# Performance work log

Measured on AMD Instinct MI355X. Metric: run time of the kernel, lower is better.

Reference implementation:

```python
import jax, jax.numpy as jnp
import numpy as np

N_ENT, N_CON, DIM, R, NB = 30000, 29309, 128, 12, 8
B, LC, S, E_DB, E_CON = 256, 50, 32, 300000, 200000


def setup_inputs() -> dict:
    key = jax.random.key(0)
    ks = jax.random.split(key, 32)
    f = lambda k, sh: (jax.random.normal(k, sh, jnp.float32) * 0.02)
    concept_emb = f(ks[0], (N_CON, DIM)).at[0].set(0.0)  # padding_idx=0 row zeroed
    inp = {
        'concept_mask': jax.random.randint(ks[1], (B, LC), 0, N_CON, jnp.int32),
        'seed_pad': jax.random.randint(ks[2], (B, S), 0, N_ENT, jnp.int32),
        'seed_lens': jax.random.randint(ks[3], (B,), 0, S + 1, jnp.int32),
        'db_edge_index': jax.random.randint(ks[4], (2, E_DB), 0, N_ENT, jnp.int32),
        'db_edge_type': jax.random.randint(ks[5], (E_DB,), 0, R, jnp.int32),
        'con_edge_index': jax.random.randint(ks[6], (2, E_CON), 0, N_CON, jnp.int32),
        'db_vec': jax.random.uniform(ks[7], (B, N_ENT), jnp.float32),
        'labels': jax.random.randint(ks[8], (B,), 0, N_ENT, jnp.int64),
        'rec': jax.random.uniform(ks[9], (B,), jnp.float32),
        'concept_emb': concept_emb,
        'basis': f(ks[10], (NB, N_ENT, DIM)),
        'comp': f(ks[11], (R, NB)),
        'rgcn_root': f(ks[12], (N_ENT, DIM)),
        'rgcn_bias': jnp.zeros((DIM,), jnp.float32),
        'gcn_w': f(ks[13], (DIM, DIM)),
        'gcn_b': jnp.zeros((DIM,), jnp.float32),
        'attn_a': f(ks[14], (DIM, DIM)),
        'attn_b': f(ks[15], (DIM, 1)),
        'attn_a_db': f(ks[16], (DIM, DIM)),
        'attn_b_db': f(ks[17], (DIM, 1)),
        'user_norm_w': f(ks[18], (DIM, 2 * DIM)),
        'user_norm_b': jnp.zeros((DIM,), jnp.float32),
        'gate_norm_w': f(ks[19], (1, DIM)),
        'gate_norm_b': jnp.zeros((1,), jnp.float32),
        'info_con_w': f(ks[20], (DIM, DIM)),
        'info_con_b': jnp.zeros((DIM,), jnp.float32),
        'info_out_db_b': jnp.zeros((N_ENT,), jnp.float32),
        'output_en_b': jnp.zeros((N_ENT,), jnp.float32),
    }
    return inp


def _forward(concept_mask, seed_pad, seed_lens, db_edge_index, db_edge_type,
             con_edge_index, db_vec, labels, rec, concept_emb, basis, comp,
             rgcn_root, rgcn_bias, gcn_w, gcn_b, attn_a, attn_b, attn_a_db,
             attn_b_db, user_norm_w, user_norm_b, gate_norm_w, gate_norm_b,
             info_con_w, info_con_b, info_out_db_b, output_en_b):
    NEG = jnp.float32(-1e30)
    # ---- RGCN over DBpedia graph (x=None -> per-edge row W[rel][src]) ----
    w = jnp.einsum('rb,bnd->rnd', comp, basis)            # [R, N_ent, D]
    src, dst = db_edge_index[0], db_edge_index[1]
    msg = w[db_edge_type, src]                            # [E, D]
    agg = jax.ops.segment_sum(msg, dst, num_segments=N_ENT)
    cnt = jax.ops.segment_sum(jnp.ones_like(dst, jnp.float32), dst, num_segments=N_ENT)
    db_feats = agg / jnp.maximum(cnt, 1.0)[:, None] + rgcn_root + rgcn_bias  # mean aggr + root + bias
    # ---- GCN over concept graph (symmetric norm, self-loops) ----
    xw = concept_emb @ gcn_w
    loops = jnp.arange(N_CON, dtype=con_edge_index.dtype)
    cs = jnp.concatenate([con_edge_index[0], loops])
    cd = jnp.concatenate([con_edge_index[1], loops])
    deg = jax.ops.segment_sum(jnp.ones_like(cd, jnp.float32), cd, num_segments=N_CON)
    dinv = jnp.where(deg > 0, jax.lax.rsqrt(jnp.maximum(deg, 1e-12)), 0.0)
    norm = dinv[cs] * dinv[cd]
    con_feats = jax.ops.segment_sum(norm[:, None] * xw[cs], cd, num_segments=N_CON) + gcn_b
    # ---- per-sample seed-set self-attention over db features ----
    h = db_feats[seed_pad]                                # [B, S, D]
    e = jnp.tanh(h @ attn_a_db) @ attn_b_db               # [B, S, 1]
    valid = jnp.arange(S)[None, :] < seed_lens[:, None]   # [B, S]
    a = jax.nn.softmax(jnp.where(valid[..., None], e, NEG), axis=1)
    db_user = jnp.einsum('bso,bsd->bd', a, h)             # weighted sum (o=1)
    has_seed = (seed_lens > 0)
    db_user = jnp.where(has_seed[:, None], db_user, 0.0)  # empty seed set -> zeros
    db_con_mask = has_seed.astype(jnp.float32)
    # ---- batch self-attention over gathered concept features ----
    hc = con_feats[concept_mask]                          # [B, LC, D]
    ec = jnp.tanh(hc @ attn_a) @ attn_b                   # [B, LC, 1]
    cvalid = (concept_mask != 0)
    ac = jax.nn.softmax(jnp.where(cvalid[..., None], ec, NEG), axis=1)
    con_user = jnp.einsum('blo,bld->bd', ac, hc)
    # ---- gated fusion ----
    u = jnp.concatenate([con_user, db_user], axis=-1) @ user_norm_w.T + user_norm_b
    gate = jax.nn.sigmoid(u @ gate_norm_w.T + gate_norm_b)  # [B, 1]
    user_emb = gate * db_user + (1.0 - gate) * con_user
    entity_scores = user_emb @ db_feats.T + output_en_b   # [B, N_ent]
    # ---- infomax MSE loss ----
    con_e = con_user @ info_con_w.T + info_con_b
    db_scores = con_e @ db_feats.T + info_out_db_b
    info_db_loss = jnp.mean(jnp.sum((db_scores - db_vec) ** 2, axis=-1) * db_con_mask)
    # ---- rec CE loss ----
    logp = jax.nn.log_softmax(entity_scores, axis=-1)
    ce = -jnp.take_along_axis(logp, labels[:, None].astype(jnp.int32), axis=1)[:, 0]
    rec_loss = jnp.sum(ce * rec)
    loss = rec_loss + 0.025 * info_db_loss                # pretrain=False path
    return loss, entity_scores, rec_loss


def reference(concept_mask, seed_pad, seed_lens, db_edge_index, db_edge_type,
              con_edge_index, db_vec, labels, rec, concept_emb, basis, comp,
              rgcn_root, rgcn_bias, gcn_w, gcn_b, attn_a, attn_b, attn_a_db,
              attn_b_db, user_norm_w, user_norm_b, gate_norm_w, gate_norm_b,
              info_con_w, info_con_b, info_out_db_b, output_en_b):
    return _forward(concept_mask, seed_pad, seed_lens, db_edge_index, db_edge_type,
                    con_edge_index, db_vec, labels, rec, concept_emb, basis, comp,
                    rgcn_root, rgcn_bias, gcn_w, gcn_b, attn_a, attn_b, attn_a_db,
                    attn_b_db, user_norm_w, user_norm_b, gate_norm_w, gate_norm_b,
                    info_con_w, info_con_b, info_out_db_b, output_en_b)
```

## Files before the change

kernel.cpp:

```cpp
#include <hip/hip_runtime.h>

#define N_ENT  30000
#define N_CON  29309
#define DIM    128
#define NBASIS 8
#define NREL   12
#define BATCH  256
#define LCON   50
#define SSEED  32
#define EDB    300000
#define ECON   200000
#define NTILE  938

#define NE4      ((N_CON * DIM) / 4)
#define NB_HIST  ((EDB + ECON + 255) / 256)
#define NB_CONV  ((NE4 + 3 * (DIM * DIM / 4) + 255) / 256)
#define NB_WCOMP ((N_ENT * 32) / 256)
#define NB_XW    ((N_CON + 127) / 128)
#define NB_RG    ((N_ENT + 3) / 4)
#define NB_GG    ((N_CON + 3) / 4)
#define NB_EDB   ((N_ENT + 31) / 32)
#define NB_ECON  ((N_CON + 31) / 32)

typedef __attribute__((ext_vector_type(8)))  short bfrag8;
typedef __attribute__((ext_vector_type(16))) float facc16;

__device__ __forceinline__ unsigned short f2bf(float f) {
    unsigned int u = __float_as_uint(f);
    u += 0x7FFFu + ((u >> 16) & 1u);
    return (unsigned short)(u >> 16);
}
__device__ __forceinline__ float bf2f(unsigned int h) {
    return __uint_as_float(h << 16);
}

__global__ __launch_bounds__(256) void prep_kernel(const int* __restrict__ db_dst,
                                                   const int* __restrict__ con_dst,
                                                   const float* __restrict__ emb,
                                                   const float* __restrict__ W,
                                                   const float* __restrict__ A_db,
                                                   const float* __restrict__ A_c,
                                                   int* __restrict__ cnt_e, int* __restrict__ cnt_c,
                                                   int* __restrict__ ord_db, int* __restrict__ ord_con,
                                                   unsigned short* __restrict__ emb_h,
                                                   unsigned short* __restrict__ Wt_h,
                                                   unsigned short* __restrict__ At_db_h,
                                                   unsigned short* __restrict__ At_c_h) {
    int t = threadIdx.x, bb = blockIdx.x;
    if (bb < NB_HIST) {
        int e = bb * 256 + t;
        if (e < EDB) {
            ord_db[e] = atomicAdd(cnt_e + db_dst[e], 1);
        } else if (e < EDB + ECON) {
            int ee = e - EDB;
            ord_con[ee] = atomicAdd(cnt_c + con_dst[ee], 1);
        }
        return;
    }
    int i = (bb - NB_HIST) * 256 + t;
    if (i < NE4) {
        float4 v = ((const float4*)emb)[i];
        unsigned int p0 = (unsigned int)f2bf(v.x) | ((unsigned int)f2bf(v.y) << 16);
        unsigned int p1 = (unsigned int)f2bf(v.z) | ((unsigned int)f2bf(v.w) << 16);
        *(uint2*)(emb_h + (size_t)i * 4) = make_uint2(p0, p1);
    } else {
        int j = i - NE4;
        if (j < 3 * (DIM * DIM) / 4) {
            int sel = j >> 12;
            int jj = j & 4095;
            const float* S = (sel == 0) ? W : ((sel == 1) ? A_db : A_c);
            unsigned short* Dst = (sel == 0) ? Wt_h : ((sel == 1) ? At_db_h : At_c_h);
            int o = jj * 4;
            int n = o >> 7, k0 = o & 127;
            unsigned int p0 = (unsigned int)f2bf(S[(k0 + 0) * DIM + n]) |
                              ((unsigned int)f2bf(S[(k0 + 1) * DIM + n]) << 16);
            unsigned int p1 = (unsigned int)f2bf(S[(k0 + 2) * DIM + n]) |
                              ((unsigned int)f2bf(S[(k0 + 3) * DIM + n]) << 16);
            *(uint2*)(Dst + n * DIM + k0) = make_uint2(p0, p1);
        }
    }
}

__device__ void scan_block(const int* __restrict__ cnt, int n, int* __restrict__ rowptr) {
    __shared__ int part[1024];
    int t = threadIdx.x;
    int per = (n + 1023) / 1024;
    int s0 = t * per;
    int sum = 0;
    for (int i = 0; i < per; ++i) {
        int idx = s0 + i;
        if (idx < n) sum += cnt[idx];
    }
    part[t] = sum;
    __syncthreads();
    for (int off = 1; off < 1024; off <<= 1) {
        int v = (t >= off) ? part[t - off] : 0;
        __syncthreads();
        part[t] += v;
        __syncthreads();
    }
    int run = part[t] - sum;
    for (int i = 0; i < per; ++i) {
        int idx = s0 + i;
        if (idx < n) {
            rowptr[idx] = run;
            run += cnt[idx];
        }
    }
    if (t == 1023) rowptr[n] = part[1023];
}

__global__ __launch_bounds__(1024) void scan2_kernel(const int* __restrict__ cnt_e,
                                                     const int* __restrict__ cnt_c,
                                                     int* __restrict__ rowptr_e,
                                                     int* __restrict__ rowptr_c,
                                                     float* __restrict__ dinv,
                                                     const unsigned short* __restrict__ emb_h,
                                                     const unsigned short* __restrict__ Wt_h,
                                                     unsigned short* __restrict__ xw_h) {
    int bb = blockIdx.x;
    if (bb == 0) {
        scan_block(cnt_e, N_ENT, rowptr_e);
        return;
    }
    if (bb == 1) {
        scan_block(cnt_c, N_CON, rowptr_c);
        for (int i = threadIdx.x; i < N_CON; i += 1024)
            dinv[i] = rsqrtf((float)(cnt_c[i] + 1));
        return;
    }
    int t = threadIdx.x;
    int wave = t >> 6, lane = t & 63;
    int m0 = (bb - 2) * 128 + (wave >> 2) * 32;
    int n0 = (wave & 3) * 32;
    int am = lane & 31, ak = (lane >> 5) * 8;
    int mrow = m0 + am;
    bool mv = mrow < N_CON;
    const unsigned short* Ar = emb_h + (size_t)mrow * DIM + ak;
    const unsigned short* Br = Wt_h + (size_t)(n0 + am) * DIM + ak;
    facc16 acc;
#pragma unroll
    for (int r = 0; r < 16; ++r) acc[r] = 0.f;
#pragma unroll
    for (int s = 0; s < 8; ++s) {
        bfrag8 a;
#pragma unroll
        for (int j = 0; j < 8; ++j) a[j] = 0;
        if (mv) a = *(const bfrag8*)(Ar + s * 16);
        bfrag8 b = *(const bfrag8*)(Br + s * 16);
        acc = __builtin_amdgcn_mfma_f32_32x32x16_bf16(a, b, acc, 0, 0, 0);
    }
    int col = lane & 31;
    int g4 = (lane >> 5) * 4;
#pragma unroll
    for (int r = 0; r < 16; ++r) {
        int m = m0 + (r & 3) + ((r >> 2) << 3) + g4;
        if (m < N_CON) xw_h[(size_t)m * DIM + n0 + col] = f2bf(acc[r]);
    }
}

__global__ __launch_bounds__(256) void scatter_kernel(const int* __restrict__ db_eidx,
                                                      const int* __restrict__ db_etype,
                                                      const int* __restrict__ con_eidx,
                                                      const int* __restrict__ ord_db,
                                                      const int* __restrict__ ord_con,
                                                      const int* __restrict__ rowptr_e,
                                                      const int* __restrict__ rowptr_c,
                                                      int* __restrict__ elist_e,
                                                      int* __restrict__ elist_c) {
    int e = blockIdx.x * 256 + threadIdx.x;
    if (e < EDB) {
        int dst = db_eidx[EDB + e];
        elist_e[rowptr_e[dst] + ord_db[e]] = db_eidx[e] | (db_etype[e] << 18);
    } else if (e < EDB + ECON) {
        int ee = e - EDB;
        int dst = con_eidx[ECON + ee];
        elist_c[rowptr_c[dst] + ord_con[ee]] = con_eidx[ee];
    }
}

__global__ __launch_bounds__(256) void wcomp_gcn_kernel(const float* __restrict__ basis,
                                                        const float* __restrict__ comp,
                                                        unsigned short* __restrict__ w_h,
                                                        int use_w,
                                                        const int* __restrict__ rowptr_c,
                                                        const int* __restrict__ elist_c,
                                                        const float* __restrict__ dinv,
                                                        const unsigned short* __restrict__ xw_h,
                                                        const float* __restrict__ gcn_b,
                                                        unsigned short* __restrict__ conf_h) {
    int t = threadIdx.x, bb = blockIdx.x;
    if (bb < NB_WCOMP) {
        __shared__ float sc[NREL * NBASIS];
        if (!use_w) return;
        if (t < NREL * NBASIS) sc[t] = comp[t];
        __syncthreads();
        int i = bb * 256 + t;
        int n = i >> 5, d4 = i & 31;
        float4 bv[NBASIS];
#pragma unroll
        for (int b = 0; b < NBASIS; ++b)
            bv[b] = ((const float4*)(basis + ((size_t)b * N_ENT + n) * DIM))[d4];
#pragma unroll
        for (int r = 0; r < NREL; ++r) {
            float4 acc = make_float4(0.f, 0.f, 0.f, 0.f);
#pragma unroll
            for (int b = 0; b < NBASIS; ++b) {
                float c = sc[r * NBASIS + b];
                acc.x += c * bv[b].x; acc.y += c * bv[b].y;
                acc.z += c * bv[b].z; acc.w += c * bv[b].w;
            }
            unsigned int p0 = (unsigned int)f2bf(acc.x) | ((unsigned int)f2bf(acc.y) << 16);
            unsigned int p1 = (unsigned int)f2bf(acc.z) | ((unsigned int)f2bf(acc.w) << 16);
            *(uint2*)(w_h + ((size_t)n * NREL + r) * DIM + d4 * 4) = make_uint2(p0, p1);
        }
        return;
    }
    int gb = bb - NB_WCOMP;
    int wid = gb * 4 + (t >> 6);
    if (wid >= N_CON) return;
    int lane = t & 63;
    int beg = rowptr_c[wid], end = rowptr_c[wid + 1];
    float a0 = 0.f, a1 = 0.f;
    int p = beg;
    for (; p + 3 < end; p += 4) {
        int s0 = elist_c[p], s1 = elist_c[p + 1], s2 = elist_c[p + 2], s3 = elist_c[p + 3];
        float n0 = dinv[s0], n1 = dinv[s1], n2 = dinv[s2], n3 = dinv[s3];
        unsigned int k0 = *(const unsigned int*)(xw_h + (size_t)s0 * DIM + lane * 2);
        unsigned int k1 = *(const unsigned int*)(xw_h + (size_t)s1 * DIM + lane * 2);
        unsigned int k2 = *(const unsigned int*)(xw_h + (size_t)s2 * DIM + lane * 2);
        unsigned int k3 = *(const unsigned int*)(xw_h + (size_t)s3 * DIM + lane * 2);
        a0 += n0 * bf2f(k0 & 0xFFFF) + n1 * bf2f(k1 & 0xFFFF) + n2 * bf2f(k2 & 0xFFFF) + n3 * bf2f(k3 & 0xFFFF);
        a1 += n0 * bf2f(k0 >> 16)    + n1 * bf2f(k1 >> 16)    + n2 * bf2f(k2 >> 16)    + n3 * bf2f(k3 >> 16);
    }
    for (; p < end; ++p) {
        int s = elist_c[p];
        float nm = dinv[s];
        unsigned int k = *(const unsigned int*)(xw_h + (size_t)s * DIM + lane * 2);
        a0 += nm * bf2f(k & 0xFFFF);
        a1 += nm * bf2f(k >> 16);
    }
    float dv = dinv[wid];
    unsigned int ks = *(const unsigned int*)(xw_h + (size_t)wid * DIM + lane * 2);
    size_t base = (size_t)wid * DIM + lane * 2;
    float f0 = dv * a0 + dv * dv * bf2f(ks & 0xFFFF) + gcn_b[lane * 2];
    float f1 = dv * a1 + dv * dv * bf2f(ks >> 16)    + gcn_b[lane * 2 + 1];
    *(unsigned int*)(conf_h + base) = (unsigned int)f2bf(f0) | ((unsigned int)f2bf(f1) << 16);
}

__device__ __forceinline__ void escore_body(const unsigned short* __restrict__ feats,
                                            const unsigned short* __restrict__ At,
                                            const float* __restrict__ v,
                                            float* __restrict__ eo,
                                            int m0, int nrow) {
    __shared__ float part[4][32];
    int t = threadIdx.x;
    int wave = t >> 6, lane = t & 63;
    int n0 = wave * 32;
    int am = lane & 31, ak = (lane >> 5) * 8;
    int mrow = m0 + am;
    bool mv = mrow < nrow;
    const unsigned short* Ar = feats + (size_t)mrow * DIM + ak;
    const unsigned short* Br = At + (size_t)(n0 + am) * DIM + ak;
    facc16 acc;
#pragma unroll
    for (int r = 0; r < 16; ++r) acc[r] = 0.f;
#pragma unroll
    for (int s = 0; s < 8; ++s) {
        bfrag8 a;
#pragma unroll
        for (int j = 0; j < 8; ++j) a[j] = 0;
        if (mv) a = *(const bfrag8*)(Ar + s * 16);
        bfrag8 b = *(const bfrag8*)(Br + s * 16);
        acc = __builtin_amdgcn_mfma_f32_32x32x16_bf16(a, b, acc, 0, 0, 0);
    }
    int col = lane & 31, g = lane >> 5;
    float vn = v[n0 + col];
#pragma unroll
    for (int r = 0; r < 16; ++r) {
        float x = tanhf(acc[r]) * vn;
#pragma unroll
        for (int off = 16; off >= 1; off >>= 1) x += __shfl_xor(x, off, 32);
        if (col == 0) {
            int row = (r & 3) + ((r >> 2) << 3) + (g << 2);
            part[wave][row] = x;
        }
    }
    __syncthreads();
    if (t < 32) {
        int m = m0 + t;
        if (m < nrow)
            eo[m] = part[0][t] + part[1][t] + part[2][t] + part[3][t];
    }
}

__global__ __launch_bounds__(256) void rgcn_escore_kernel(const int* __restrict__ rowptr_e,
                                                          const int* __restrict__ elist_e,
                                                          const unsigned short* __restrict__ w_h,
                                                          const float* __restrict__ root,
                                                          const float* __restrict__ bias,
                                                          unsigned short* __restrict__ dbf_h,
                                                          const unsigned short* __restrict__ conf_h,
                                                          const unsigned short* __restrict__ At_c_h,
                                                          const float* __restrict__ v_c,
                                                          float* __restrict__ e_con,
                                                          int use_w) {
    int bb = blockIdx.x;
    if (bb < NB_RG) {
        if (!use_w) return;
        int wid = bb * 4 + (threadIdx.x >> 6);
        int lane = threadIdx.x & 63;
        int beg = rowptr_e[wid], end = rowptr_e[wid + 1];
        float a0 = 0.f, a1 = 0.f;
        int p = beg;
        for (; p + 3 < end; p += 4) {
            int v0 = elist_e[p], v1 = elist_e[p + 1], v2 = elist_e[p + 2], v3 = elist_e[p + 3];
            unsigned int k0 = *(const unsigned int*)(w_h + ((size_t)(v0 & 0x3FFFF) * NREL + (v0 >> 18)) * DIM + lane * 2);
            unsigned int k1 = *(const unsigned int*)(w_h + ((size_t)(v1 & 0x3FFFF) * NREL + (v1 >> 18)) * DIM + lane * 2);
            unsigned int k2 = *(const unsigned int*)(w_h + ((size_t)(v2 & 0x3FFFF) * NREL + (v2 >> 18)) * DIM + lane * 2);
            unsigned int k3 = *(const unsigned int*)(w_h + ((size_t)(v3 & 0x3FFFF) * NREL + (v3 >> 18)) * DIM + lane * 2);
            a0 += bf2f(k0 & 0xFFFF) + bf2f(k1 & 0xFFFF) + bf2f(k2 & 0xFFFF) + bf2f(k3 & 0xFFFF);
            a1 += bf2f(k0 >> 16)    + bf2f(k1 >> 16)    + bf2f(k2 >> 16)    + bf2f(k3 >> 16);
        }
        for (; p < end; ++p) {
            int v = elist_e[p];
            unsigned int k = *(const unsigned int*)(w_h + ((size_t)(v & 0x3FFFF) * NREL + (v >> 18)) * DIM + lane * 2);
            a0 += bf2f(k & 0xFFFF);
            a1 += bf2f(k >> 16);
        }
        float inv = 1.f / fmaxf((float)(end - beg), 1.f);
        size_t base = (size_t)wid * DIM + lane * 2;
        float f0 = a0 * inv + root[base]     + bias[lane * 2];
        float f1 = a1 * inv + root[base + 1] + bias[lane * 2 + 1];
        *(unsigned int*)(dbf_h + base) = (unsigned int)f2bf(f0) | ((unsigned int)f2bf(f1) << 16);
        return;
    }
    escore_body(conf_h, At_c_h, v_c, e_con, (bb - NB_RG) * 32, N_CON);
}

__global__ __launch_bounds__(256) void rgcn_gather_basis(const int* __restrict__ rowptr,
                                                         const int* __restrict__ elist,
                                                         const float* __restrict__ basis,
                                                         const float* __restrict__ comp,
                                                         const float* __restrict__ root,
                                                         const float* __restrict__ bias,
                                                         unsigned short* __restrict__ dbf_h) {
    int wid  = blockIdx.x * 4 + (threadIdx.x >> 6);
    int lane = threadIdx.x & 63;
    if (wid >= N_ENT) return;
    int beg = rowptr[wid], end = rowptr[wid + 1];
    float a0 = 0.f, a1 = 0.f;
    for (int p = beg; p < end; ++p) {
        int v = elist[p];
        int src = v & 0x3FFFF, ty = v >> 18;
        const float* c = comp + ty * NBASIS;
#pragma unroll
        for (int b = 0; b < NBASIS; ++b) {
            const float* bp = basis + ((size_t)b * N_ENT + src) * DIM;
            a0 += c[b] * bp[lane * 2];
            a1 += c[b] * bp[lane * 2 + 1];
        }
    }
    float inv = 1.f / fmaxf((float)(end - beg), 1.f);
    size_t base = (size_t)wid * DIM + lane * 2;
    float f0 = a0 * inv + root[base]     + bias[lane * 2];
    float f1 = a1 * inv + root[base + 1] + bias[lane * 2 + 1];
    *(unsigned int*)(dbf_h + base) = (unsigned int)f2bf(f0) | ((unsigned int)f2bf(f1) << 16);
}

__global__ __launch_bounds__(256) void escore_db_kernel(const unsigned short* __restrict__ dbf_h,
                                                        const unsigned short* __restrict__ At_db_h,
                                                        const float* __restrict__ v_db,
                                                        float* __restrict__ e_db) {
    escore_body(dbf_h, At_db_h, v_db, e_db, blockIdx.x * 32, N_ENT);
}

__global__ __launch_bounds__(256) void attn_fusion_kernel(const unsigned short* __restrict__ dbf_h,
                                                          const unsigned short* __restrict__ conf_h,
                                                          const float* __restrict__ e_db,
                                                          const float* __restrict__ e_con,
                                                          const int* __restrict__ seed_pad,
                                                          const int* __restrict__ seed_lens,
                                                          const int* __restrict__ concept_mask,
                                                          const float* __restrict__ Wu, const float* __restrict__ bu,
                                                          const float* __restrict__ gw, const float* __restrict__ gb,
                                                          const float* __restrict__ Wi, const float* __restrict__ bi,
                                                          unsigned short* __restrict__ uemb_h,
                                                          unsigned short* __restrict__ cone_h,
                                                          float* __restrict__ maskv) {
    __shared__ int srow[SSEED];
    __shared__ int crow[LCON];
    __shared__ float a_db[SSEED], a_con[LCON];
    __shared__ float du[DIM], cu[DIM], red[DIM];
    int b = blockIdx.x, t = threadIdx.x;
    int wave = t >> 6, lane = t & 63;
    int len = seed_lens[b];
    if (wave == 0) {
        float e = -1e30f;
        if (lane < SSEED) {
            int rv = seed_pad[b * SSEED + lane];
            srow[lane] = rv;
            if (lane < len) e = e_db[rv];
        }
        float m = e;
#pragma unroll
        for (int off = 16; off >= 1; off >>= 1) m = fmaxf(m, __shfl_xor(m, off, 32));
        float p = (lane < SSEED) ? __expf(e - m) : 0.f;
        float s = p;
#pragma unroll
        for (int off = 16; off >= 1; off >>= 1) s += __shfl_xor(s, off, 32);
        if (lane < SSEED) a_db[lane] = p / s;
    } else if (wave == 1) {
        float e = -1e30f;
        if (lane < LCON) {
            int rv = concept_mask[b * LCON + lane];
            crow[lane] = rv;
            if (rv != 0) e = e_con[rv];
        }
        float m = e;
#pragma unroll
        for (int off = 32; off >= 1; off >>= 1) m = fmaxf(m, __shfl_xor(m, off, 64));
        float p = (lane < LCON) ? __expf(e - m) : 0.f;
        float s = p;
#pragma unroll
        for (int off = 32; off >= 1; off >>= 1) s += __shfl_xor(s, off, 64);
        if (lane < LCON) a_con[lane] = p / s;
    }
    __syncthreads();
    if (t < DIM) {
        float acc = 0.f;
#pragma unroll
        for (int s = 0; s < SSEED; ++s)
            acc += a_db[s] * bf2f((unsigned int)dbf_h[(size_t)srow[s] * DIM + t]);
        du[t] = (len > 0) ? acc : 0.f;
    } else {
        int d = t - DIM;
        float acc = 0.f;
#pragma unroll
        for (int s = 0; s < LCON; ++s)
            acc += a_con[s] * bf2f((unsigned int)conf_h[(size_t)crow[s] * DIM + d]);
        cu[d] = acc;
    }
    __syncthreads();
    if (t < DIM) {
        float u = bu[t];
        const float* wr = Wu + t * 2 * DIM;
        for (int k = 0; k < DIM; ++k) u += cu[k] * wr[k];
        for (int k = 0; k < DIM; ++k) u += du[k] * wr[DIM + k];
        red[t] = u * gw[t];
    }
    __syncthreads();
    for (int s2 = 64; s2 > 0; s2 >>= 1) {
        if (t < s2) red[t] += red[t + s2];
        __syncthreads();
    }
    if (t < DIM) {
        float gate = 1.f / (1.f + __expf(-(red[0] + gb[0])));
        uemb_h[b * DIM + t] = f2bf(gate * du[t] + (1.f - gate) * cu[t]);
        float ce = bi[t];
        const float* wi = Wi + t * DIM;
        for (int k = 0; k < DIM; ++k) ce += cu[k] * wi[k];
        cone_h[b * DIM + t] = f2bf(ce);
    }
    if (t == 0) maskv[b] = (len > 0) ? 1.f : 0.f;
}

__global__ __launch_bounds__(256) void score_mfma(const unsigned short* __restrict__ dbf_h,
                                                  const unsigned short* __restrict__ uemb_h,
                                                  const unsigned short* __restrict__ cone_h,
                                                  const float* __restrict__ en_b,
                                                  const float* __restrict__ info_b,
                                                  const float* __restrict__ db_vec,
                                                  float* __restrict__ escore,
                                                  float* __restrict__ partM,
                                                  float* __restrict__ partS,
                                                  float* __restrict__ partQ) {
    int wave = threadIdx.x >> 6, lane = threadIdx.x & 63;
    int nt = blockIdx.x * 4 + wave;
    if (nt >= NTILE) return;
    int b0 = blockIdx.y * 32;
    int n0 = nt * 32;
    int am = lane & 31, ak = (lane >> 5) * 8;
    int nb = n0 + am;
    bool bvalid = nb < N_ENT;
    const unsigned short* Au = uemb_h + (size_t)(b0 + am) * DIM + ak;
    const unsigned short* Ac = cone_h + (size_t)(b0 + am) * DIM + ak;
    const unsigned short* Bp = dbf_h + (size_t)nb * DIM + ak;
    facc16 accE, accD;
#pragma unroll
    for (int r = 0; r < 16; ++r) { accE[r] = 0.f; accD[r] = 0.f; }
#pragma unroll
    for (int s = 0; s < 8; ++s) {
        bfrag8 au = *(const bfrag8*)(Au + s * 16);
        bfrag8 ac = *(const bfrag8*)(Ac + s * 16);
        bfrag8 bb;
#pragma unroll
        for (int j = 0; j < 8; ++j) bb[j] = 0;
        if (bvalid) bb = *(const bfrag8*)(Bp + s * 16);
        accE = __builtin_amdgcn_mfma_f32_32x32x16_bf16(au, bb, accE, 0, 0, 0);
        accD = __builtin_amdgcn_mfma_f32_32x32x16_bf16(ac, bb, accD, 0, 0, 0);
    }
    int col = lane & 31;
    int n = n0 + col;
    bool nv = n < N_ENT;
    float enb = nv ? en_b[n] : 0.f;
    float inb = nv ? info_b[n] : 0.f;
    int g4 = (lane >> 5) * 4;
#pragma unroll
    for (int r = 0; r < 16; ++r) {
        int b = b0 + (r & 3) + ((r >> 2) << 3) + g4;
        float e = accE[r] + enb;
        if (nv) escore[(size_t)b * N_ENT + n] = e;
        float ev = nv ? e : -1e30f;
        float mx = ev;
#pragma unroll
        for (int off = 16; off >= 1; off >>= 1) mx = fmaxf(mx, __shfl_xor(mx, off, 64));
        float ex = nv ? __expf(e - mx) : 0.f;
        float sm = ex;
#pragma unroll
        for (int off = 16; off >= 1; off >>= 1) sm += __shfl_xor(sm, off, 64);
        float d = nv ? (accD[r] + inb - db_vec[(size_t)b * N_ENT + n]) : 0.f;
        float q = d * d;
#pragma unroll
        for (int off = 16; off >= 1; off >>= 1) q += __shfl_xor(q, off, 64);
        if (col == 0) {
            partM[(size_t)b * NTILE + nt] = mx;
            partS[(size_t)b * NTILE + nt] = sm;
            partQ[(size_t)b * NTILE + nt] = q;
        }
    }
}

__global__ __launch_bounds__(256) void ce_final(const float* __restrict__ partM,
                                                const float* __restrict__ partS,
                                                const float* __restrict__ partQ,
                                                const float* __restrict__ escore,
                                                const int* __restrict__ labels,
                                                const float* __restrict__ rec,
                                                float* __restrict__ rloss,
                                                float* __restrict__ ssqv) {
    __shared__ float red[256], red2[256];
    int b = blockIdx.x, t = threadIdx.x;
    const float* pm = partM + (size_t)b * NTILE;
    const float* ps = partS + (size_t)b * NTILE;
    const float* pq = partQ + (size_t)b * NTILE;
    float mx = -1e30f;
    for (int i = t; i < NTILE; i += 256) mx = fmaxf(mx, pm[i]);
    red[t] = mx;
    __syncthreads();
    for (int s2 = 128; s2 > 0; s2 >>= 1) {
        if (t < s2) red[t] = fmaxf(red[t], red[t + s2]);
        __syncthreads();
    }
    float M = red[0];
    __syncthreads();
    float s = 0.f, q = 0.f;
    for (int i = t; i < NTILE; i += 256) {
        s += ps[i] * __expf(pm[i] - M);
        q += pq[i];
    }
    red[t] = s; red2[t] = q;
    __syncthreads();
    for (int s2 = 128; s2 > 0; s2 >>= 1) {
        if (t < s2) { red[t] += red[t + s2]; red2[t] += red2[t + s2]; }
        __syncthreads();
    }
    if (t == 0) {
        float lse = M + logf(red[0]);
        float ce  = -(escore[(size_t)b * N_ENT + labels[b]] - lse);
        rloss[b]  = ce * rec[b];
        ssqv[b]   = red2[0];
    }
}

__global__ __launch_bounds__(256) void final_kernel(const float* __restrict__ rloss,
                                                    const float* __restrict__ sumsq,
                                                    const float* __restrict__ maskv,
                                                    float* __restrict__ out) {
    __shared__ float r1[256], r2[256];
    int t = threadIdx.x;
    r1[t] = rloss[t];
    r2[t] = sumsq[t] * maskv[t];
    __syncthreads();
    for (int s2 = 128; s2 > 0; s2 >>= 1) {
        if (t < s2) { r1[t] += r1[t + s2]; r2[t] += r2[t + s2]; }
        __syncthreads();
    }
    if (t == 0) {
        float rec_loss = r1[0];
        float info = r2[0] / (float)BATCH;
        out[0] = rec_loss + 0.025f * info;
        out[1 + (size_t)BATCH * N_ENT] = rec_loss;
    }
}

extern "C" void kernel_launch(void* const* d_in, const int* in_sizes, int n_in,
                              void* d_out, int out_size, void* d_ws, size_t ws_size,
                              hipStream_t stream) {
    (void)in_sizes; (void)n_in; (void)out_size;
    const int*   concept_mask  = (const int*)d_in[0];
    const int*   seed_pad      = (const int*)d_in[1];
    const int*   seed_lens     = (const int*)d_in[2];
    const int*   db_eidx       = (const int*)d_in[3];
    const int*   db_etype      = (const int*)d_in[4];
    const int*   con_eidx      = (const int*)d_in[5];
    const float* db_vec        = (const float*)d_in[6];
    const int*   labels        = (const int*)d_in[7];
    const float* rec           = (const float*)d_in[8];
    const float* concept_emb   = (const float*)d_in[9];
    const float* basis         = (const float*)d_in[10];
    const float* comp          = (const float*)d_in[11];
    const float* rgcn_root     = (const float*)d_in[12];
    const float* rgcn_bias     = (const float*)d_in[13];
    const float* gcn_w         = (const float*)d_in[14];
    const float* gcn_b         = (const float*)d_in[15];
    const float* attn_a        = (const float*)d_in[16];
    const float* attn_b        = (const float*)d_in[17];
    const float* attn_a_db     = (const float*)d_in[18];
    const float* attn_b_db     = (const float*)d_in[19];
    const float* user_norm_w   = (const float*)d_in[20];
    const float* user_norm_b   = (const float*)d_in[21];
    const float* gate_norm_w   = (const float*)d_in[22];
    const float* gate_norm_b   = (const float*)d_in[23];
    const float* info_con_w    = (const float*)d_in[24];
    const float* info_con_b    = (const float*)d_in[25];
    const float* info_out_db_b = (const float*)d_in[26];
    const float* output_en_b   = (const float*)d_in[27];

    float* ws = (float*)d_ws;
    size_t off = 0;
    auto alloc = [&](size_t n) { float* p = ws + off; off += (n + 255) & ~(size_t)255; return p; };
    float* dinv   = alloc(N_CON);
    float* maskv  = alloc(BATCH);
    float* rls    = alloc(BATCH);
    float* ssqv   = alloc(BATCH);
    float* partM  = alloc((size_t)BATCH * NTILE);
    float* partS  = alloc((size_t)BATCH * NTILE);
    float* partQ  = alloc((size_t)BATCH * NTILE);
    int* cnt_e    = (int*)alloc(N_ENT + N_CON);
    int* cnt_c    = cnt_e + N_ENT;
    int* rowptr_e = (int*)alloc(N_ENT + 1);
    int* rowptr_c = (int*)alloc(N_CON + 1);
    int* ord_db   = (int*)alloc(EDB);
    int* ord_con  = (int*)alloc(ECON);
    int* elist_e  = (int*)alloc(EDB);
    int* elist_c  = (int*)alloc(ECON);
    unsigned short* dbf_h  = (unsigned short*)alloc((size_t)N_ENT * DIM / 2);
    unsigned short* conf_h = (unsigned short*)alloc((size_t)N_CON * DIM / 2 + 128);
    unsigned short* xw_h   = (unsigned short*)alloc((size_t)N_CON * DIM / 2 + 128);
    unsigned short* emb_h  = (unsigned short*)alloc((size_t)N_CON * DIM / 2 + 128);
    unsigned short* Wt_h   = (unsigned short*)alloc(DIM * DIM / 2);
    unsigned short* uemb_h = (unsigned short*)alloc(BATCH * DIM / 2);
    unsigned short* cone_h = (unsigned short*)alloc(BATCH * DIM / 2);
    float* e_db   = alloc(N_ENT);
    float* e_con  = alloc(N_CON);
    unsigned short* At_db_h = (unsigned short*)alloc(DIM * DIM / 2);
    unsigned short* At_c_h  = (unsigned short*)alloc(DIM * DIM / 2);
    size_t w_elems = ((size_t)NREL * N_ENT * DIM) / 2;
    int use_w = (off + w_elems) * sizeof(float) <= ws_size;
    unsigned short* w_h = (unsigned short*)(ws + off);

    float* out    = (float*)d_out;
    float* escore = out + 1;

    (void)hipMemsetAsync(cnt_e, 0, (N_ENT + N_CON) * sizeof(int), stream);

    prep_kernel<<<NB_HIST + NB_CONV, 256, 0, stream>>>(
        db_eidx + EDB, con_eidx + ECON, concept_emb, gcn_w, attn_a_db, attn_a,
        cnt_e, cnt_c, ord_db, ord_con, emb_h, Wt_h, At_db_h, At_c_h);
    scan2_kernel<<<2 + NB_XW, 1024, 0, stream>>>(cnt_e, cnt_c, rowptr_e, rowptr_c, dinv,
                                                 emb_h, Wt_h, xw_h);
    scatter_kernel<<<NB_HIST, 256, 0, stream>>>(db_eidx, db_etype, con_eidx,
                                                ord_db, ord_con, rowptr_e, rowptr_c,
                                                elist_e, elist_c);
    wcomp_gcn_kernel<<<NB_WCOMP + NB_GG, 256, 0, stream>>>(basis, comp, w_h, use_w,
                                                           rowptr_c, elist_c, dinv, xw_h,
                                                           gcn_b, conf_h);
    if (!use_w) {
        rgcn_gather_basis<<<NB_RG, 256, 0, stream>>>(rowptr_e, elist_e, basis, comp,
                                                     rgcn_root, rgcn_bias, dbf_h);
    }
    rgcn_escore_kernel<<<NB_RG + NB_ECON, 256, 0, stream>>>(rowptr_e, elist_e, w_h,
                                                            rgcn_root, rgcn_bias, dbf_h,
                                                            conf_h, At_c_h, attn_b, e_con, use_w);
    escore_db_kernel<<<NB_EDB, 256, 0, stream>>>(dbf_h, At_db_h, attn_b_db, e_db);
    attn_fusion_kernel<<<BATCH, 256, 0, stream>>>(dbf_h, conf_h, e_db, e_con,
                                                  seed_pad, seed_lens, concept_mask,
                                                  user_norm_w, user_norm_b, gate_norm_w, gate_norm_b,
                                                  info_con_w, info_con_b, uemb_h, cone_h, maskv);
    dim3 sg((NTILE + 3) / 4, BATCH / 32);
    score_mfma<<<sg, 256, 0, stream>>>(dbf_h, uemb_h, cone_h, output_en_b, info_out_db_b, db_vec,
                                       escore, partM, partS, partQ);
    ce_final<<<BATCH, 256, 0, stream>>>(partM, partS, partQ, escore, labels, rec, rls, ssqv);
    final_kernel<<<1, 256, 0, stream>>>(rls, ssqv, maskv, out);
}
```

Before: 516.4 us.

## Regroup kernels so basis compose runs in prep and gathers pair together

Moves the relation-weight composition (basis x comp) into the prep kernel, interleaving its blocks with histogram and bf16 conversion blocks. The RGCN gather and GCN gather become one kernel with alternating block roles, and the two attention-score MFMA passes become a second interleaved kernel. This removes one launch, lets independent streaming and atomic work share the GPU, and places each gather next to its partner. In exchange the weight composition now runs before the scan and scatter, and the extra shared memory plus branching in prep may lower occupancy.

```diff
diff --git a/kernel.cpp b/kernel.cpp
--- a/kernel.cpp
+++ b/kernel.cpp
@@ -16,6 +16,7 @@
 #define NB_HIST  ((EDB + ECON + 255) / 256)
 #define NB_CONV  ((NE4 + 3 * (DIM * DIM / 4) + 255) / 256)
 #define NB_WCOMP ((N_ENT * 32) / 256)
+#define NB_PREP  (NB_HIST * 5)
 #define NB_XW    ((N_CON + 127) / 128)
 #define NB_RG    ((N_ENT + 3) / 4)
 #define NB_GG    ((N_CON + 3) / 4)
@@ -40,15 +41,21 @@
                                                    const float* __restrict__ W,
                                                    const float* __restrict__ A_db,
                                                    const float* __restrict__ A_c,
+                                                   const float* __restrict__ basis,
+                                                   const float* __restrict__ comp,
                                                    int* __restrict__ cnt_e, int* __restrict__ cnt_c,
                                                    int* __restrict__ ord_db, int* __restrict__ ord_con,
                                                    unsigned short* __restrict__ emb_h,
                                                    unsigned short* __restrict__ Wt_h,
                                                    unsigned short* __restrict__ At_db_h,
-                                                   unsigned short* __restrict__ At_c_h) {
+                                                   unsigned short* __restrict__ At_c_h,
+                                                   unsigned short* __restrict__ w_h,
+                                                   int use_w) {
+    __shared__ float sc[NREL * NBASIS];
     int t = threadIdx.x, bb = blockIdx.x;
-    if (bb < NB_HIST) {
-        int e = bb * 256 + t;
+    int g = bb / 5, slot = bb % 5;
+    if (slot == 0) {
+        int e = g * 256 + t;
         if (e < EDB) {
             ord_db[e] = atomicAdd(cnt_e + db_dst[e], 1);
         } else if (e < EDB + ECON) {
@@ -57,27 +64,56 @@
         }
         return;
     }
-    int i = (bb - NB_HIST) * 256 + t;
-    if (i < NE4) {
-        float4 v = ((const float4*)emb)[i];
-        unsigned int p0 = (unsigned int)f2bf(v.x) | ((unsigned int)f2bf(v.y) << 16);
-        unsigned int p1 = (unsigned int)f2bf(v.z) | ((unsigned int)f2bf(v.w) << 16);
-        *(uint2*)(emb_h + (size_t)i * 4) = make_uint2(p0, p1);
-    } else {
-        int j = i - NE4;
-        if (j < 3 * (DIM * DIM) / 4) {
-            int sel = j >> 12;
-            int jj = j & 4095;
-            const float* S = (sel == 0) ? W : ((sel == 1) ? A_db : A_c);
-            unsigned short* Dst = (sel == 0) ? Wt_h : ((sel == 1) ? At_db_h : At_c_h);
-            int o = jj * 4;
-            int n = o >> 7, k0 = o & 127;
-            unsigned int p0 = (unsigned int)f2bf(S[(k0 + 0) * DIM + n]) |
-                              ((unsigned int)f2bf(S[(k0 + 1) * DIM + n]) << 16);
-            unsigned int p1 = (unsigned int)f2bf(S[(k0 + 2) * DIM + n]) |
-                              ((unsigned int)f2bf(S[(k0 + 3) * DIM + n]) << 16);
-            *(uint2*)(Dst + n * DIM + k0) = make_uint2(p0, p1);
-        }
+    if (slot <= 2) {
+        int cb = g * 2 + (slot - 1);
+        if (cb >= NB_CONV) return;
+        int i = cb * 256 + t;
+        if (i < NE4) {
+            float4 v = ((const float4*)emb)[i];
+            unsigned int p0 = (unsigned int)f2bf(v.x) | ((unsigned int)f2bf(v.y) << 16);
+            unsigned int p1 = (unsigned int)f2bf(v.z) | ((unsigned int)f2bf(v.w) << 16);
+            *(uint2*)(emb_h + (size_t)i * 4) = make_uint2(p0, p1);
+        } else {
+            int j = i - NE4;
+            if (j < 3 * (DIM * DIM) / 4) {
+                int sel = j >> 12;
+                int jj = j & 4095;
+                const float* S = (sel == 0) ? W : ((sel == 1) ? A_db : A_c);
+                unsigned short* Dst = (sel == 0) ? Wt_h : ((sel == 1) ? At_db_h : At_c_h);
+                int o = jj * 4;
+                int n = o >> 7, k0 = o & 127;
+                unsigned int p0 = (unsigned int)f2bf(S[(k0 + 0) * DIM + n]) |
+                                  ((unsigned int)f2bf(S[(k0 + 1) * DIM + n]) << 16);
+                unsigned int p1 = (unsigned int)f2bf(S[(k0 + 2) * DIM + n]) |
+                                  ((unsigned int)f2bf(S[(k0 + 3) * DIM + n]) << 16);
+                *(uint2*)(Dst + n * DIM + k0) = make_uint2(p0, p1);
+            }
+        }
+        return;
+    }
+    if (!use_w) return;
+    int wb = g * 2 + (slot - 3);
+    if (wb >= NB_WCOMP) return;
+    if (t < NREL * NBASIS) sc[t] = comp[t];
+    __syncthreads();
+    int i = wb * 256 + t;
+    int n = i >> 5, d4 = i & 31;
+    float4 bv[NBASIS];
+#pragma unroll
+    for (int b = 0; b < NBASIS; ++b)
+        bv[b] = ((const float4*)(basis + ((size_t)b * N_ENT + n) * DIM))[d4];
+#pragma unroll
+    for (int r = 0; r < NREL; ++r) {
+        float4 acc = make_float4(0.f, 0.f, 0.f, 0.f);
+#pragma unroll
+        for (int b = 0; b < NBASIS; ++b) {
+            float c = sc[r * NBASIS + b];
+            acc.x += c * bv[b].x; acc.y += c * bv[b].y;
+            acc.z += c * bv[b].z; acc.w += c * bv[b].w;
+        }
+        unsigned int p0 = (unsigned int)f2bf(acc.x) | ((unsigned int)f2bf(acc.y) << 16);
+        unsigned int p1 = (unsigned int)f2bf(acc.z) | ((unsigned int)f2bf(acc.w) << 16);
+        *(uint2*)(w_h + ((size_t)n * NREL + r) * DIM + d4 * 4) = make_uint2(p0, p1);
     }
 }
 
@@ -179,47 +215,53 @@
     }
 }
 
-__global__ __launch_bounds__(256) void wcomp_gcn_kernel(const float* __restrict__ basis,
-                                                        const float* __restrict__ comp,
-                                                        unsigned short* __restrict__ w_h,
-                                                        int use_w,
-                                                        const int* __restrict__ rowptr_c,
-                                                        const int* __restrict__ elist_c,
-                                                        const float* __restrict__ dinv,
-                                                        const unsigned short* __restrict__ xw_h,
-                                                        const float* __restrict__ gcn_b,
-                                                        unsigned short* __restrict__ conf_h) {
-    int t = threadIdx.x, bb = blockIdx.x;
-    if (bb < NB_WCOMP) {
-        __shared__ float sc[NREL * NBASIS];
+__global__ __launch_bounds__(256) void gathers_kernel(const int* __restrict__ rowptr_e,
+                                                      const int* __restrict__ elist_e,
+                                                      const unsigned short* __restrict__ w_h,
+                                                      const float* __restrict__ root,
+                                                      const float* __restrict__ bias,
+                                                      unsigned short* __restrict__ dbf_h,
+                                                      const int* __restrict__ rowptr_c,
+                                                      const int* __restrict__ elist_c,
+                                                      const float* __restrict__ dinv,
+                                                      const unsigned short* __restrict__ xw_h,
+                                                      const float* __restrict__ gcn_b,
+                                                      unsigned short* __restrict__ conf_h,
+                                                      int use_w) {
+    int bb = blockIdx.x;
+    int pair = bb >> 1;
+    int lane = threadIdx.x & 63;
+    if ((bb & 1) == 0) {
         if (!use_w) return;
-        if (t < NREL * NBASIS) sc[t] = comp[t];
-        __syncthreads();
-        int i = bb * 256 + t;
-        int n = i >> 5, d4 = i & 31;
-        float4 bv[NBASIS];
-#pragma unroll
-        for (int b = 0; b < NBASIS; ++b)
-            bv[b] = ((const float4*)(basis + ((size_t)b * N_ENT + n) * DIM))[d4];
-#pragma unroll
-        for (int r = 0; r < NREL; ++r) {
-            float4 acc = make_float4(0.f, 0.f, 0.f, 0.f);
-#pragma unroll
-            for (int b = 0; b < NBASIS; ++b) {
-                float c = sc[r * NBASIS + b];
-                acc.x += c * bv[b].x; acc.y += c * bv[b].y;
-                acc.z += c * bv[b].z; acc.w += c * bv[b].w;
-            }
-            unsigned int p0 = (unsigned int)f2bf(acc.x) | ((unsigned int)f2bf(acc.y) << 16);
-            unsigned int p1 = (unsigned int)f2bf(acc.z) | ((unsigned int)f2bf(acc.w) << 16);
-            *(uint2*)(w_h + ((size_t)n * NREL + r) * DIM + d4 * 4) = make_uint2(p0, p1);
-        }
+        int wid = pair * 4 + (threadIdx.x >> 6);
+        int beg = rowptr_e[wid], end = rowptr_e[wid + 1];
+        float a0 = 0.f, a1 = 0.f;
+        int p = beg;
+        for (; p + 3 < end; p += 4) {
+            int v0 = elist_e[p], v1 = elist_e[p + 1], v2 = elist_e[p + 2], v3 = elist_e[p + 3];
+            unsigned int k0 = *(const unsigned int*)(w_h + ((size_t)(v0 & 0x3FFFF) * NREL + (v0 >> 18)) * DIM + lane * 2);
+            unsigned int k1 = *(const unsigned int*)(w_h + ((size_t)(v1 & 0x3FFFF) * NREL + (v1 >> 18)) * DIM + lane * 2);
+            unsigned int k2 = *(const unsigned int*)(w_h + ((size_t)(v2 & 0x3FFFF) * NREL + (v2 >> 18)) * DIM + lane * 2);
+            unsigned int k3 = *(const unsigned int*)(w_h + ((size_t)(v3 & 0x3FFFF) * NREL + (v3 >> 18)) * DIM + lane * 2);
+            a0 += bf2f(k0 & 0xFFFF) + bf2f(k1 & 0xFFFF) + bf2f(k2 & 0xFFFF) + bf2f(k3 & 0xFFFF);
+            a1 += bf2f(k0 >> 16)    + bf2f(k1 >> 16)    + bf2f(k2 >> 16)    + bf2f(k3 >> 16);
+        }
+        for (; p < end; ++p) {
+            int v = elist_e[p];
+            unsigned int k = *(const unsigned int*)(w_h + ((size_t)(v & 0x3FFFF) * NREL + (v >> 18)) * DIM + lane * 2);
+            a0 += bf2f(k & 0xFFFF);
+            a1 += bf2f(k >> 16);
+        }
+        float inv = 1.f / fmaxf((float)(end - beg), 1.f);
+        size_t base = (size_t)wid * DIM + lane * 2;
+        float f0 = a0 * inv + root[base]     + bias[lane * 2];
+        float f1 = a1 * inv + root[base + 1] + bias[lane * 2 + 1];
+        *(unsigned int*)(dbf_h + base) = (unsigned int)f2bf(f0) | ((unsigned int)f2bf(f1) << 16);
         return;
     }
-    int gb = bb - NB_WCOMP;
-    int wid = gb * 4 + (t >> 6);
+    if (pair >= NB_GG) return;
+    int wid = pair * 4 + (threadIdx.x >> 6);
     if (wid >= N_CON) return;
-    int lane = t & 63;
     int beg = rowptr_c[wid], end = rowptr_c[wid + 1];
     float a0 = 0.f, a1 = 0.f;
     int p = beg;
@@ -246,96 +288,6 @@
     float f0 = dv * a0 + dv * dv * bf2f(ks & 0xFFFF) + gcn_b[lane * 2];
     float f1 = dv * a1 + dv * dv * bf2f(ks >> 16)    + gcn_b[lane * 2 + 1];
     *(unsigned int*)(conf_h + base) = (unsigned int)f2bf(f0) | ((unsigned int)f2bf(f1) << 16);
-}
-
-__device__ __forceinline__ void escore_body(const unsigned short* __restrict__ feats,
-                                            const unsigned short* __restrict__ At,
-                                            const float* __restrict__ v,
-                                            float* __restrict__ eo,
-                                            int m0, int nrow) {
-    __shared__ float part[4][32];
-    int t = threadIdx.x;
-    int wave = t >> 6, lane = t & 63;
-    int n0 = wave * 32;
-    int am = lane & 31, ak = (lane >> 5) * 8;
-    int mrow = m0 + am;
-    bool mv = mrow < nrow;
-    const unsigned short* Ar = feats + (size_t)mrow * DIM + ak;
-    const unsigned short* Br = At + (size_t)(n0 + am) * DIM + ak;
-    facc16 acc;
-#pragma unroll
-    for (int r = 0; r < 16; ++r) acc[r] = 0.f;
-#pragma unroll
-    for (int s = 0; s < 8; ++s) {
-        bfrag8 a;
-#pragma unroll
-        for (int j = 0; j < 8; ++j) a[j] = 0;
-        if (mv) a = *(const bfrag8*)(Ar + s * 16);
-        bfrag8 b = *(const bfrag8*)(Br + s * 16);
-        acc = __builtin_amdgcn_mfma_f32_32x32x16_bf16(a, b, acc, 0, 0, 0);
-    }
-    int col = lane & 31, g = lane >> 5;
-    float vn = v[n0 + col];
-#pragma unroll
-    for (int r = 0; r < 16; ++r) {
-        float x = tanhf(acc[r]) * vn;
-#pragma unroll
-        for (int off = 16; off >= 1; off >>= 1) x += __shfl_xor(x, off, 32);
-        if (col == 0) {
-            int row = (r & 3) + ((r >> 2) << 3) + (g << 2);
-            part[wave][row] = x;
-        }
-    }
-    __syncthreads();
-    if (t < 32) {
-        int m = m0 + t;
-        if (m < nrow)
-            eo[m] = part[0][t] + part[1][t] + part[2][t] + part[3][t];
-    }
-}
-
-__global__ __launch_bounds__(256) void rgcn_escore_kernel(const int* __restrict__ rowptr_e,
-                                                          const int* __restrict__ elist_e,
-                                                          const unsigned short* __restrict__ w_h,
-                                                          const float* __restrict__ root,
-                                                          const float* __restrict__ bias,
-                                                          unsigned short* __restrict__ dbf_h,
-                                                          const unsigned short* __restrict__ conf_h,
-                                                          const unsigned short* __restrict__ At_c_h,
-                                                          const float* __restrict__ v_c,
-                                                          float* __restrict__ e_con,
-                                                          int use_w) {
-    int bb = blockIdx.x;
-    if (bb < NB_RG) {
-        if (!use_w) return;
-        int wid = bb * 4 + (threadIdx.x >> 6);
-        int lane = threadIdx.x & 63;
-        int beg = rowptr_e[wid], end = rowptr_e[wid + 1];
-        float a0 = 0.f, a1 = 0.f;
-        int p = beg;
-        for (; p + 3 < end; p += 4) {
-            int v0 = elist_e[p], v1 = elist_e[p + 1], v2 = elist_e[p + 2], v3 = elist_e[p + 3];
-            unsigned int k0 = *(const unsigned int*)(w_h + ((size_t)(v0 & 0x3FFFF) * NREL + (v0 >> 18)) * DIM + lane * 2);
-            unsigned int k1 = *(const unsigned int*)(w_h + ((size_t)(v1 & 0x3FFFF) * NREL + (v1 >> 18)) * DIM + lane * 2);
-            unsigned int k2 = *(const unsigned int*)(w_h + ((size_t)(v2 & 0x3FFFF) * NREL + (v2 >> 18)) * DIM + lane * 2);
-            unsigned int k3 = *(const unsigned int*)(w_h + ((size_t)(v3 & 0x3FFFF) * NREL + (v3 >> 18)) * DIM + lane * 2);
-            a0 += bf2f(k0 & 0xFFFF) + bf2f(k1 & 0xFFFF) + bf2f(k2 & 0xFFFF) + bf2f(k3 & 0xFFFF);
-            a1 += bf2f(k0 >> 16)    + bf2f(k1 >> 16)    + bf2f(k2 >> 16)    + bf2f(k3 >> 16);
-        }
-        for (; p < end; ++p) {
-            int v = elist_e[p];
-            unsigned int k = *(const unsigned int*)(w_h + ((size_t)(v & 0x3FFFF) * NREL + (v >> 18)) * DIM + lane * 2);
-            a0 += bf2f(k & 0xFFFF);
-            a1 += bf2f(k >> 16);
-        }
-        float inv = 1.f / fmaxf((float)(end - beg), 1.f);
-        size_t base = (size_t)wid * DIM + lane * 2;
-        float f0 = a0 * inv + root[base]     + bias[lane * 2];
-        float f1 = a1 * inv + root[base + 1] + bias[lane * 2 + 1];
-        *(unsigned int*)(dbf_h + base) = (unsigned int)f2bf(f0) | ((unsigned int)f2bf(f1) << 16);
-        return;
-    }
-    escore_body(conf_h, At_c_h, v_c, e_con, (bb - NB_RG) * 32, N_CON);
 }
 
 __global__ __launch_bounds__(256) void rgcn_gather_basis(const int* __restrict__ rowptr,
@@ -368,11 +320,69 @@
     *(unsigned int*)(dbf_h + base) = (unsigned int)f2bf(f0) | ((unsigned int)f2bf(f1) << 16);
 }
 
-__global__ __launch_bounds__(256) void escore_db_kernel(const unsigned short* __restrict__ dbf_h,
-                                                        const unsigned short* __restrict__ At_db_h,
-                                                        const float* __restrict__ v_db,
-                                                        float* __restrict__ e_db) {
-    escore_body(dbf_h, At_db_h, v_db, e_db, blockIdx.x * 32, N_ENT);
+__device__ __forceinline__ void escore_body(const unsigned short* __restrict__ feats,
+                                            const unsigned short* __restrict__ At,
+                                            const float* __restrict__ v,
+                                            float* __restrict__ eo,
+                                            int m0, int nrow) {
+    __shared__ float part[4][32];
+    int t = threadIdx.x;
+    int wave = t >> 6, lane = t & 63;
+    int n0 = wave * 32;
+    int am = lane & 31, ak = (lane >> 5) * 8;
+    int mrow = m0 + am;
+    bool mv = mrow < nrow;
+    const unsigned short* Ar = feats + (size_t)mrow * DIM + ak;
+    const unsigned short* Br = At + (size_t)(n0 + am) * DIM + ak;
+    facc16 acc;
+#pragma unroll
+    for (int r = 0; r < 16; ++r) acc[r] = 0.f;
+#pragma unroll
+    for (int s = 0; s < 8; ++s) {
+        bfrag8 a;
+#pragma unroll
+        for (int j = 0; j < 8; ++j) a[j] = 0;
+        if (mv) a = *(const bfrag8*)(Ar + s * 16);
+        bfrag8 b = *(const bfrag8*)(Br + s * 16);
+        acc = __builtin_amdgcn_mfma_f32_32x32x16_bf16(a, b, acc, 0, 0, 0);
+    }
+    int col = lane & 31, g = lane >> 5;
+    float vn = v[n0 + col];
+#pragma unroll
+    for (int r = 0; r < 16; ++r) {
+        float x = tanhf(acc[r]) * vn;
+#pragma unroll
+        for (int off = 16; off >= 1; off >>= 1) x += __shfl_xor(x, off, 32);
+        if (col == 0) {
+            int row = (r & 3) + ((r >> 2) << 3) + (g << 2);
+            part[wave][row] = x;
+        }
+    }
+    __syncthreads();
+    if (t < 32) {
+        int m = m0 + t;
+        if (m < nrow)
+            eo[m] = part[0][t] + part[1][t] + part[2][t] + part[3][t];
+    }
+}
+
+__global__ __launch_bounds__(256) void escores_kernel(const unsigned short* __restrict__ dbf_h,
+                                                      const unsigned short* __restrict__ At_db_h,
+                                                      const float* __restrict__ v_db,
+                                                      float* __restrict__ e_db,
+                                                      const unsigned short* __restrict__ conf_h,
+                                                      const unsigned short* __restrict__ At_c_h,
+                                                      const float* __restrict__ v_c,
+                                                      float* __restrict__ e_con) {
+    int bb = blockIdx.x;
+    int pair = bb >> 1;
+    if ((bb & 1) == 0) {
+        if (pair >= NB_EDB) return;
+        escore_body(dbf_h, At_db_h, v_db, e_db, pair * 32, N_ENT);
+    } else {
+        if (pair >= NB_ECON) return;
+        escore_body(conf_h, At_c_h, v_c, e_con, pair * 32, N_CON);
+    }
 }
 
 __global__ __launch_bounds__(256) void attn_fusion_kernel(const unsigned short* __restrict__ dbf_h,
@@ -665,25 +675,24 @@
 
     (void)hipMemsetAsync(cnt_e, 0, (N_ENT + N_CON) * sizeof(int), stream);
 
-    prep_kernel<<<NB_HIST + NB_CONV, 256, 0, stream>>>(
+    prep_kernel<<<NB_PREP, 256, 0, stream>>>(
         db_eidx + EDB, con_eidx + ECON, concept_emb, gcn_w, attn_a_db, attn_a,
-        cnt_e, cnt_c, ord_db, ord_con, emb_h, Wt_h, At_db_h, At_c_h);
+        basis, comp, cnt_e, cnt_c, ord_db, ord_con, emb_h, Wt_h, At_db_h, At_c_h,
+        w_h, use_w);
     scan2_kernel<<<2 + NB_XW, 1024, 0, stream>>>(cnt_e, cnt_c, rowptr_e, rowptr_c, dinv,
                                                  emb_h, Wt_h, xw_h);
     scatter_kernel<<<NB_HIST, 256, 0, stream>>>(db_eidx, db_etype, con_eidx,
                                                 ord_db, ord_con, rowptr_e, rowptr_c,
                                                 elist_e, elist_c);
-    wcomp_gcn_kernel<<<NB_WCOMP + NB_GG, 256, 0, stream>>>(basis, comp, w_h, use_w,
-                                                           rowptr_c, elist_c, dinv, xw_h,
-                                                           gcn_b, conf_h);
+    gathers_kernel<<<NB_RG * 2, 256, 0, stream>>>(rowptr_e, elist_e, w_h, rgcn_root, rgcn_bias,
+                                                  dbf_h, rowptr_c, elist_c, dinv, xw_h, gcn_b,
+                                                  conf_h, use_w);
     if (!use_w) {
         rgcn_gather_basis<<<NB_RG, 256, 0, stream>>>(rowptr_e, elist_e, basis, comp,
                                                      rgcn_root, rgcn_bias, dbf_h);
     }
-    rgcn_escore_kernel<<<NB_RG + NB_ECON, 256, 0, stream>>>(rowptr_e, elist_e, w_h,
-                                                            rgcn_root, rgcn_bias, dbf_h,
-                                                            conf_h, At_c_h, attn_b, e_con, use_w);
-    escore_db_kernel<<<NB_EDB, 256, 0, stream>>>(dbf_h, At_db_h, attn_b_db, e_db);
+    escores_kernel<<<NB_EDB * 2, 256, 0, stream>>>(dbf_h, At_db_h, attn_b_db, e_db,
+                                                   conf_h, At_c_h, attn_b, e_con);
     attn_fusion_kernel<<<BATCH, 256, 0, stream>>>(dbf_h, conf_h, e_db, e_con,
                                                   seed_pad, seed_lens, concept_mask,
                                                   user_norm_w, user_norm_b, gate_norm_w, gate_norm_b,
```

After: 506.9 us. Within noise of the previous version (-1.8%).
